# Optimization experiments

Measured on AMD Instinct MI355X. Metric: run time of the kernel, lower is better.

## Reference

```python
import jax, jax.numpy as jnp
import numpy as np

B, N, F, K = 4, 512, 128, 32
GAMMA = 10.0          # RBF width parameter
CUTOFF = 5.0          # RBF center range [0, CUTOFF]
LOG2 = 0.6931471805599453
EPS = 1e-12           # keeps sqrt grad finite on the (masked-out) diagonal


def ssp(x):
    # shifted softplus: ln(0.5*e^x + 0.5) = softplus(x) - ln 2
    return jax.nn.softplus(x) - LOG2


def setup_inputs() -> dict:
    key = jax.random.key(0)
    ks = jax.random.split(key, 8)
    coordinates = jax.random.normal(ks[0], (B, N, 3), dtype=jnp.float32) * 3.0
    atom_emb = jax.random.normal(ks[1], (B, N, F), dtype=jnp.float32)
    rbf_centers = jnp.linspace(0.0, CUTOFF, K, dtype=jnp.float32)
    # cfconv filter-generator dense layers
    w1 = jax.random.normal(ks[2], (K, F), dtype=jnp.float32) / np.float32(np.sqrt(K))
    b1 = jnp.zeros((F,), dtype=jnp.float32)
    w2 = jax.random.normal(ks[3], (F, F), dtype=jnp.float32) / np.float32(np.sqrt(F))
    b2 = jnp.zeros((F,), dtype=jnp.float32)
    # self.W linear (nn.Linear stores weight as [out, in])
    Ww = jax.random.normal(ks[4], (F, F), dtype=jnp.float32) / np.float32(np.sqrt(F))
    Wb = jnp.zeros((F,), dtype=jnp.float32)
    return {"coordinates": coordinates, "atom_emb": atom_emb,
            "rbf_centers": rbf_centers, "w1": w1, "b1": b1,
            "w2": w2, "b2": b2, "Ww": Ww, "Wb": Wb}


def reference(coordinates, atom_emb, rbf_centers, w1, b1, w2, b2, Ww, Wb):
    n = coordinates.shape[-2]
    # pairwise distances [B, N, N]
    diff = coordinates[:, :, None, :] - coordinates[:, None, :, :]
    d = jnp.sqrt(jnp.sum(diff * diff, axis=-1) + EPS)
    # Gaussian RBF expansion [B, N, N, K]
    rbf = jnp.exp(-GAMMA * (d[..., None] - rbf_centers) ** 2)
    # filter generator: Dense -> SSP -> Dense -> SSP  => W [B, N, N, F]
    Wf = ssp(jnp.einsum('bnmk,kf->bnmf', rbf, w1) + b1)
    Wf = ssp(jnp.einsum('bnmf,fg->bnmg', Wf, w2) + b2)
    # zero the diagonal (no self-interaction)
    mask = (1.0 - jnp.eye(n, dtype=Wf.dtype))[None, :, :, None]
    Wf = Wf * mask
    # x = self.W(atom_emb)
    x = atom_emb @ Ww.T + Wb
    # per-channel weighted neighbor aggregation
    x = jnp.einsum('bnmf,bmf->bnf', Wf, x)
    return atom_emb + x
```

## Files before the change

### kernel.cpp

```cpp
#include <hip/hip_runtime.h>
#include <hip/hip_bf16.h>

#define B_ 4
#define N_ 512
#define F_ 128
#define K_ 32
#define TD 2048
#define DMAX 6.5f
#define XWB (B_ * N_ / 2)
#define TKEEPI 1890

typedef __attribute__((ext_vector_type(4))) float f32x4;

__device__ __forceinline__ unsigned cvt_pk_bf16(float a, float b) {
  unsigned r;
  asm("v_cvt_pk_bf16_f32 %0, %1, %2" : "=v"(r) : "v"(a), "v"(b));
  return r;
}
__device__ __forceinline__ unsigned short f2bf1(float a) {
  return (unsigned short)cvt_pk_bf16(a, a);
}
__device__ __forceinline__ float exp2_hw(float x) {
  float r; asm("v_exp_f32 %0, %1" : "=v"(r) : "v"(x)); return r;
}
__device__ __forceinline__ float log2_hw(float x) {
  float r; asm("v_log_f32 %0, %1" : "=v"(r) : "v"(x)); return r;
}
__device__ __forceinline__ float lo16f(unsigned w) {
  return __builtin_bit_cast(float, w << 16);
}
__device__ __forceinline__ float hi16f(unsigned w) {
  return __builtin_bit_cast(float, w & 0xffff0000u);
}

__device__ __forceinline__ float sspb(float u) {
  float e = exp2_hw(__builtin_fabsf(u) * -1.4426950408889634f);
  float l = log2_hw(fmaf(e, 0.5f, 0.5f));
  return fmaf(l, 0.6931471805599453f, fmaxf(u, 0.f));
}

__launch_bounds__(256)
__global__ void prep_kernel(const float* __restrict__ emb, const float* __restrict__ Ww,
                            const float* __restrict__ Wb,
                            const float* __restrict__ w1, const float* __restrict__ b1,
                            const float* __restrict__ w2, const float* __restrict__ b2,
                            unsigned short* __restrict__ xbf,
                            unsigned short* __restrict__ tabn) {
  __shared__ float erow[2][F_];
  __shared__ float rbf_s[2][K_];
  __shared__ float h1s[2][F_];

  if (blockIdx.x < XWB) {
    const int r0 = blockIdx.x * 2;
    const int half = threadIdx.x >> 7, f = threadIdx.x & 127;
    erow[half][f] = emb[(r0 + half) * F_ + f];
    __syncthreads();
    const float4* w4 = (const float4*)(Ww + f * F_);
    const float* er = erow[half];
    float acc = 0.f;
#pragma unroll 8
    for (int g4 = 0; g4 < F_ / 4; ++g4) {
      float4 wv = w4[g4];
      acc = fmaf(er[g4 * 4 + 0], wv.x, acc);
      acc = fmaf(er[g4 * 4 + 1], wv.y, acc);
      acc = fmaf(er[g4 * 4 + 2], wv.z, acc);
      acc = fmaf(er[g4 * 4 + 3], wv.w, acc);
    }
    xbf[(r0 + half) * F_ + f] = f2bf1(acc + Wb[f]);
  } else {
    const int j = blockIdx.x - XWB;
    const int sl = threadIdx.x >> 7, f = threadIdx.x & 127;
    const int i = 2 * j + sl;
    const float d = (float)i * (DMAX / (float)(TD - 1));
    if (f < K_) {
      float t = d - (float)f * (5.0f / 31.0f);
      rbf_s[sl][f] = exp2_hw(t * t * -14.426950408889634f);
    }
    __syncthreads();
    float a1 = b1[f];
#pragma unroll 8
    for (int k = 0; k < K_; ++k) a1 = fmaf(rbf_s[sl][k], w1[k * F_ + f], a1);
    h1s[sl][f] = sspb(a1);
    __syncthreads();
    float a2 = b2[f];
#pragma unroll 8
    for (int g = 0; g < F_; ++g) a2 = fmaf(h1s[sl][g], w2[g * F_ + f], a2);
    tabn[i * F_ + f] = f2bf1(sspb(a2));
  }
}

__launch_bounds__(256, 6)
__global__ void agg_kernel(const float* __restrict__ coords, const float* __restrict__ emb,
                           const unsigned short* __restrict__ xbf,
                           const unsigned short* __restrict__ tabn,
                           float* __restrict__ out) {
  __shared__ unsigned tci[N_];
  __shared__ unsigned cidx[N_ + 80];
  __shared__ unsigned cnt_s;
  __shared__ float part[16][F_ + 4];

  const int blk = blockIdx.x;
  const int b = blk >> 9, n = blk & 511;
  const int tid = threadIdx.x;
  const int lane = tid & 63;

  const float cx = coords[(b * N_ + n) * 3 + 0];
  const float cy = coords[(b * N_ + n) * 3 + 1];
  const float cz = coords[(b * N_ + n) * 3 + 2];

  const float SC = (float)(TD - 1) / DMAX;
  for (int m = tid; m < N_; m += 256) {
    const float* cm = coords + (b * N_ + m) * 3;
    float dx = cm[0] - cx, dy = cm[1] - cy, dz = cm[2] - cz;
    float d = sqrtf(fmaf(dx, dx, fmaf(dy, dy, fmaf(dz, dz, 1e-12f))));
    int ti = (int)fminf(fmaf(d, SC, 0.5f), (float)(TD - 1));
    tci[m] = ((unsigned)ti << 16) | (unsigned)m;
  }
  __syncthreads();

  if (tid < 64) {
    unsigned base = 0;
#pragma unroll 1
    for (int chunk = 0; chunk < N_ / 64; ++chunk) {
      int m = chunk * 64 + lane;
      unsigned v = tci[m];
      bool keep = ((v >> 16) < TKEEPI) && (m != n);
      unsigned long long msk = __ballot(keep);
      unsigned pos = base + (unsigned)__popcll(msk & ((1ull << lane) - 1ull));
      if (keep) cidx[pos] = v;
      base += (unsigned)__popcll(msk);
    }
    cidx[base + lane] = ((unsigned)(TD - 1)) << 16;
    if (lane == 0) cnt_s = base;
  }
  __syncthreads();
  const int cnt = (int)cnt_s;

  const int mg = tid >> 4;
  const int f0 = (tid & 15) * 8;
  const unsigned short* xp = xbf + b * N_ * F_ + f0;
  const unsigned short* tp = tabn + f0;

  f32x4 acc0 = {0.f, 0.f, 0.f, 0.f};
  f32x4 acc1 = {0.f, 0.f, 0.f, 0.f};

#define LOADP(V, T, X)                                                       \
  {                                                                          \
    unsigned v_ = (V);                                                       \
    T = *(const uint4*)(tp + (v_ >> 16) * F_);                               \
    X = *(const uint4*)(xp + (v_ & 0xffffu) * F_);                           \
  }
#define MAC8(T, X)                                                           \
  {                                                                          \
    acc0[0] = fmaf(lo16f(T.x), lo16f(X.x), acc0[0]);                         \
    acc0[1] = fmaf(hi16f(T.x), hi16f(X.x), acc0[1]);                         \
    acc0[2] = fmaf(lo16f(T.y), lo16f(X.y), acc0[2]);                         \
    acc0[3] = fmaf(hi16f(T.y), hi16f(X.y), acc0[3]);                         \
    acc1[0] = fmaf(lo16f(T.z), lo16f(X.z), acc1[0]);                         \
    acc1[1] = fmaf(hi16f(T.z), hi16f(X.z), acc1[1]);                         \
    acc1[2] = fmaf(lo16f(T.w), lo16f(X.w), acc1[2]);                         \
    acc1[3] = fmaf(hi16f(T.w), hi16f(X.w), acc1[3]);                         \
  }

  uint4 tA, xA, tB, xB;
  LOADP(cidx[mg], tA, xA)
  LOADP(cidx[mg + 16], tB, xB)
  int k = mg;
#pragma unroll 1
  while (k < cnt) {
    int kn = k + 32;
    uint4 tC, xC, tD, xD;
    LOADP(cidx[kn], tC, xC)
    LOADP(cidx[kn + 16], tD, xD)
    MAC8(tA, xA)
    MAC8(tB, xB)
    k = kn;
    tA = tC; xA = xC; tB = tD; xB = xD;
  }
#undef LOADP
#undef MAC8

  *(f32x4*)&part[mg][f0] = acc0;
  *(f32x4*)&part[mg][f0 + 4] = acc1;
  __syncthreads();

  if (tid < F_) {
    float s = 0.f;
#pragma unroll
    for (int g = 0; g < 16; ++g) s += part[g][tid];
    int o = (b * N_ + n) * F_ + tid;
    out[o] = emb[o] + s;
  }
}

extern "C" void kernel_launch(void* const* d_in, const int* in_sizes, int n_in,
                              void* d_out, int out_size, void* d_ws, size_t ws_size,
                              hipStream_t stream) {
  const float* coords = (const float*)d_in[0];
  const float* emb    = (const float*)d_in[1];
  const float* w1 = (const float*)d_in[3];
  const float* b1 = (const float*)d_in[4];
  const float* w2 = (const float*)d_in[5];
  const float* b2 = (const float*)d_in[6];
  const float* Ww = (const float*)d_in[7];
  const float* Wb = (const float*)d_in[8];
  float* out = (float*)d_out;

  unsigned short* xbf  = (unsigned short*)d_ws;
  unsigned short* tabn = xbf + B_ * N_ * F_;

  hipLaunchKernelGGL(prep_kernel, dim3(XWB + TD / 2), dim3(256), 0, stream,
                     emb, Ww, Wb, w1, b1, w2, b2, xbf, tabn);
  hipLaunchKernelGGL(agg_kernel, dim3(B_ * N_), dim3(256), 0, stream,
                     coords, emb, xbf, tabn, out);
}
```

Measured before the change: 39.45 us.

## Parallelize neighbor compaction across waves and deepen gather prefetch pipeline

The neighbor-list compaction used to run serially in a single wave over 8 chunks. It now computes distances in registers, and all four waves do their ballots in parallel, with the offsets coming from a small per-wave count array. The serial tail and the staging LDS array are gone. The gather loop also prefetches two iterations ahead instead of one to hide more memory latency. In exchange it uses more registers, so launch bounds drop to 5 waves per SIMD and sentinel padding grows to 96 entries.

Result: no change. 39.09 us (median of 2 runs) (-0.9%).

```diff
diff --git a/kernel.cpp b/kernel.cpp
--- a/kernel.cpp
+++ b/kernel.cpp
@@ -89,52 +89,61 @@
   }
 }
 
-__launch_bounds__(256, 6)
+__launch_bounds__(256, 5)
 __global__ void agg_kernel(const float* __restrict__ coords, const float* __restrict__ emb,
                            const unsigned short* __restrict__ xbf,
                            const unsigned short* __restrict__ tabn,
                            float* __restrict__ out) {
-  __shared__ unsigned tci[N_];
-  __shared__ unsigned cidx[N_ + 80];
-  __shared__ unsigned cnt_s;
+  __shared__ unsigned cidx[N_ + 96];
+  __shared__ unsigned wcnt[4];
   __shared__ float part[16][F_ + 4];
 
   const int blk = blockIdx.x;
   const int b = blk >> 9, n = blk & 511;
   const int tid = threadIdx.x;
-  const int lane = tid & 63;
+  const int lane = tid & 63, wq = tid >> 6;
 
   const float cx = coords[(b * N_ + n) * 3 + 0];
   const float cy = coords[(b * N_ + n) * 3 + 1];
   const float cz = coords[(b * N_ + n) * 3 + 2];
 
   const float SC = (float)(TD - 1) / DMAX;
-  for (int m = tid; m < N_; m += 256) {
-    const float* cm = coords + (b * N_ + m) * 3;
+  const int mA = wq * 128 + lane;
+  const int mB = mA + 64;
+  unsigned vA, vB;
+  bool keepA, keepB;
+  {
+    const float* cm = coords + (b * N_ + mA) * 3;
     float dx = cm[0] - cx, dy = cm[1] - cy, dz = cm[2] - cz;
     float d = sqrtf(fmaf(dx, dx, fmaf(dy, dy, fmaf(dz, dz, 1e-12f))));
     int ti = (int)fminf(fmaf(d, SC, 0.5f), (float)(TD - 1));
-    tci[m] = ((unsigned)ti << 16) | (unsigned)m;
-  }
+    vA = ((unsigned)ti << 16) | (unsigned)mA;
+    keepA = (ti < TKEEPI) && (mA != n);
+  }
+  {
+    const float* cm = coords + (b * N_ + mB) * 3;
+    float dx = cm[0] - cx, dy = cm[1] - cy, dz = cm[2] - cz;
+    float d = sqrtf(fmaf(dx, dx, fmaf(dy, dy, fmaf(dz, dz, 1e-12f))));
+    int ti = (int)fminf(fmaf(d, SC, 0.5f), (float)(TD - 1));
+    vB = ((unsigned)ti << 16) | (unsigned)mB;
+    keepB = (ti < TKEEPI) && (mB != n);
+  }
+  unsigned long long bA = __ballot(keepA);
+  unsigned long long bB = __ballot(keepB);
+  if (lane == 0) wcnt[wq] = (unsigned)(__popcll(bA) + __popcll(bB));
   __syncthreads();
-
-  if (tid < 64) {
-    unsigned base = 0;
-#pragma unroll 1
-    for (int chunk = 0; chunk < N_ / 64; ++chunk) {
-      int m = chunk * 64 + lane;
-      unsigned v = tci[m];
-      bool keep = ((v >> 16) < TKEEPI) && (m != n);
-      unsigned long long msk = __ballot(keep);
-      unsigned pos = base + (unsigned)__popcll(msk & ((1ull << lane) - 1ull));
-      if (keep) cidx[pos] = v;
-      base += (unsigned)__popcll(msk);
-    }
-    cidx[base + lane] = ((unsigned)(TD - 1)) << 16;
-    if (lane == 0) cnt_s = base;
+  const unsigned c0 = wcnt[0], c1 = wcnt[1], c2 = wcnt[2], c3 = wcnt[3];
+  const int cnt = (int)(c0 + c1 + c2 + c3);
+  {
+    unsigned pre = (wq > 0 ? c0 : 0u) + (wq > 1 ? c1 : 0u) + (wq > 2 ? c2 : 0u);
+    unsigned long long below = (1ull << lane) - 1ull;
+    unsigned posA = pre + (unsigned)__popcll(bA & below);
+    unsigned posB = pre + (unsigned)__popcll(bA) + (unsigned)__popcll(bB & below);
+    if (keepA) cidx[posA] = vA;
+    if (keepB) cidx[posB] = vB;
+    if (tid < 96) cidx[cnt + tid] = ((unsigned)(TD - 1)) << 16;
   }
   __syncthreads();
-  const int cnt = (int)cnt_s;
 
   const int mg = tid >> 4;
   const int f0 = (tid & 15) * 8;
@@ -162,20 +171,22 @@
     acc1[3] = fmaf(hi16f(T.w), hi16f(X.w), acc1[3]);                         \
   }
 
-  uint4 tA, xA, tB, xB;
+  uint4 tA, xA, tB, xB, tC, xC, tD, xD;
   LOADP(cidx[mg], tA, xA)
   LOADP(cidx[mg + 16], tB, xB)
+  LOADP(cidx[mg + 32], tC, xC)
+  LOADP(cidx[mg + 48], tD, xD)
   int k = mg;
 #pragma unroll 1
   while (k < cnt) {
-    int kn = k + 32;
-    uint4 tC, xC, tD, xD;
-    LOADP(cidx[kn], tC, xC)
-    LOADP(cidx[kn + 16], tD, xD)
+    uint4 tE, xE, tF, xF;
+    LOADP(cidx[k + 64], tE, xE)
+    LOADP(cidx[k + 80], tF, xF)
     MAC8(tA, xA)
     MAC8(tB, xB)
-    k = kn;
     tA = tC; xA = xC; tB = tD; xB = xD;
+    tC = tE; xC = xE; tD = tF; xD = xF;
+    k += 32;
   }
 #undef LOADP
 #undef MAC8
```
